# Kernel optimization log

Hardware: AMD Instinct MI355X
Metric: run time of the kernel (lower is better)

Reference implementation:

```python
import jax, jax.numpy as jnp
import numpy as np

ATTENTION_HEAD = 16
EXPANSION_LENGTH = 300
TEXT_EMBEDDING_DIM = 768
LN_EPS = 1e-3  # keras LayerNormalization default epsilon


def setup_inputs() -> dict:
    key = jax.random.key(0)
    ks = jax.random.split(key, 8)
    B, L, D = 8, 2048, TEXT_EMBEDDING_DIM
    H = ATTENTION_HEAD
    E = EXPANSION_LENGTH
    dh = D // H
    glorot = lambda k, shape, fan_in, fan_out: jax.random.uniform(
        k, shape, jnp.float32,
        -jnp.sqrt(6.0 / (fan_in + fan_out)), jnp.sqrt(6.0 / (fan_in + fan_out)))
    return {
        "q": jax.random.normal(ks[0], (B, 1, L, D), jnp.float32),
        "k": jax.random.normal(ks[1], (B, 1, L, D), jnp.float32),
        "v": jax.random.normal(ks[2], (B, 1, L, D), jnp.float32),
        "Wq": glorot(ks[3], (D, D), D, D),
        "bq": jnp.zeros((D,), jnp.float32),
        "Wv": glorot(ks[4], (D, D), D, D),
        "bv": jnp.zeros((D,), jnp.float32),
        "memory": glorot(ks[5], (E, H, dh), E, dh),
        "gamma": jnp.ones((D,), jnp.float32),
        "beta": jnp.zeros((D,), jnp.float32),
    }


def reference(q, k, v, Wq, bq, Wv, bv, memory, gamma, beta):
    B, _, L, D = q.shape
    H = ATTENTION_HEAD
    dh = D // H
    # Dense projections (v is unused by the original module)
    Q_ = q @ Wq + bq                      # (B,1,L,D)
    V_ = k @ Wv + bv                      # (B,1,L,D)
    Q = Q_.reshape(B, L, H, dh)
    V = V_.reshape(B, L, H, dh)
    # memory-query scores, ReLU instead of softmax
    eij = jax.nn.relu(jnp.einsum('ehd,blhd->belh', memory, Q))  # (B,E,L,H)
    out1 = jnp.einsum('belh,blhd->behd', eij, V)                # (B,E,H,dh)
    out2 = jnp.einsum('behd,belh->blhd', out1, eij)             # (B,L,H,dh)
    x = out2.reshape(B, 1, L, D)
    mean = jnp.mean(x, axis=-1, keepdims=True)
    var = jnp.var(x, axis=-1, keepdims=True)
    return (x - mean) * jax.lax.rsqrt(var + LN_EPS) * gamma + beta
```

## Files before the change

kernel.cpp:

```cpp
#include <hip/hip_runtime.h>
#include <hip/hip_bf16.h>
#include <stdint.h>

#define B_   8
#define L_   2048
#define D_   768
#define H_   16
#define DH   48
#define E_   300
#define EP   320
#define KP   64
#define ACH  4
#define N1T  (128 * DH * EP)

typedef __bf16 bf16;
typedef __bf16 bf16x8 __attribute__((ext_vector_type(8)));
typedef __bf16 bf16x4 __attribute__((ext_vector_type(4)));
typedef float  f32x4  __attribute__((ext_vector_type(4)));

typedef const __attribute__((address_space(1))) uint32_t guint;
typedef __attribute__((address_space(3))) uint32_t luint;

__device__ __forceinline__ f32x4 mfma16(bf16x8 a, bf16x8 b, f32x4 c) {
  return __builtin_amdgcn_mfma_f32_16x16x32_bf16(a, b, c, 0, 0, 0);
}

__global__ __launch_bounds__(256) void k_wt(const float* __restrict__ Wq,
                                            const float* __restrict__ Wv,
                                            bf16* __restrict__ WqT,
                                            bf16* __restrict__ WvT) {
  int idx = blockIdx.x * 256 + threadIdx.x;
  int n = idx / D_, k = idx % D_;
  const float* W = blockIdx.y ? Wv : Wq;
  bf16* WT = blockIdx.y ? WvT : WqT;
  WT[n * D_ + k] = (bf16)W[k * D_ + n];
}

__global__ __launch_bounds__(256) void k_mem(const float* __restrict__ M,
                                             bf16* __restrict__ MP) {
  int idx = blockIdx.x * 256 + threadIdx.x;
  int h = idx / (EP * KP);
  int r = idx % (EP * KP);
  int e = r / KP, d = r % KP;
  float v = (e < E_ && d < DH) ? M[(e * H_ + h) * DH + d] : 0.f;
  MP[idx] = (bf16)v;
}

__global__ __launch_bounds__(512, 4) void k_gemm(
    const float* __restrict__ A0, const float* __restrict__ A1,
    const bf16* __restrict__ WT0, const bf16* __restrict__ WT1,
    const float* __restrict__ b0, const float* __restrict__ b1,
    bf16* __restrict__ outQ, bf16* __restrict__ outVT) {
  __shared__ bf16 As[128 * 32];
  __shared__ bf16 Bs[256 * 32];
  const int tid = threadIdx.x, lane = tid & 63, w = tid >> 6;
  const int wr = w >> 2, wc = w & 3;
  const int lr = lane & 15, lq = lane >> 4;
  const int bid = blockIdx.x;
  const int j = (bid & 7) * 48 + (bid >> 3);
  const int n0 = (j % 3) * 256, m0 = (j / 3) * 128;
  const int mode = blockIdx.y;
  const float* A = mode ? A1 : A0;
  const bf16* WT = mode ? WT1 : WT0;
  const float* bias = mode ? b1 : b0;

  const int arow = tid >> 2, ac8 = tid & 3;
  const int aslot = ac8 ^ ((arow >> 1) & 3);

  f32x4 acc[4][4] = {};

  for (int k0 = 0; k0 < D_; k0 += 32) {
    __syncthreads();
    {
      const float* src = A + (size_t)(m0 + arow) * D_ + k0 + ac8 * 8;
      float4 f0 = *(const float4*)src;
      float4 f1 = *(const float4*)(src + 4);
      bf16x8 v;
      v[0] = (bf16)f0.x; v[1] = (bf16)f0.y; v[2] = (bf16)f0.z; v[3] = (bf16)f0.w;
      v[4] = (bf16)f1.x; v[5] = (bf16)f1.y; v[6] = (bf16)f1.z; v[7] = (bf16)f1.w;
      *(bf16x8*)&As[arow * 32 + aslot * 8] = v;
    }
#pragma unroll
    for (int t = 0; t < 2; ++t) {
      int idx = tid + t * 512;
      int brow = idx >> 2, bt = idx & 3;
      int bc8 = bt ^ ((brow >> 1) & 3);
      const bf16* src = WT + (size_t)(n0 + brow) * D_ + k0 + bc8 * 8;
      __builtin_amdgcn_global_load_lds((guint*)src,
                                       (luint*)&Bs[(t * 512 + w * 64) * 8], 16, 0, 0);
    }
    __syncthreads();
    bf16x8 af[4], bfr[4];
#pragma unroll
    for (int mi = 0; mi < 4; ++mi) {
      int row = wr * 64 + mi * 16 + lr;
      af[mi] = *(const bf16x8*)&As[row * 32 + (lq ^ ((row >> 1) & 3)) * 8];
    }
#pragma unroll
    for (int ni = 0; ni < 4; ++ni) {
      int row = wc * 64 + ni * 16 + lr;
      bfr[ni] = *(const bf16x8*)&Bs[row * 32 + (lq ^ ((row >> 1) & 3)) * 8];
    }
#pragma unroll
    for (int mi = 0; mi < 4; ++mi)
#pragma unroll
      for (int ni = 0; ni < 4; ++ni)
        acc[mi][ni] = mfma16(af[mi], bfr[ni], acc[mi][ni]);
  }

  float bs[4];
#pragma unroll
  for (int ni = 0; ni < 4; ++ni) bs[ni] = bias[n0 + wc * 64 + ni * 16 + lr];

  if (mode == 0) {
#pragma unroll
    for (int mi = 0; mi < 4; ++mi)
#pragma unroll
      for (int ni = 0; ni < 4; ++ni) {
        int m = m0 + wr * 64 + mi * 16 + lq * 4;
        int n = n0 + wc * 64 + ni * 16 + lr;
#pragma unroll
        for (int r = 0; r < 4; ++r)
          outQ[(size_t)(m + r) * D_ + n] = (bf16)(acc[mi][ni][r] + bs[ni]);
      }
  } else {
#pragma unroll
    for (int mi = 0; mi < 4; ++mi)
#pragma unroll
      for (int ni = 0; ni < 4; ++ni) {
        int mb = m0 + wr * 64 + mi * 16 + lq * 4;
        int n = n0 + wc * 64 + ni * 16 + lr;
        int bhd = (mb >> 11) * H_ + n / DH;
        int d = n % DH;
        int l = mb & (L_ - 1);
        bf16x4 v;
#pragma unroll
        for (int r = 0; r < 4; ++r) v[r] = (bf16)(acc[mi][ni][r] + bs[ni]);
        *(bf16x4*)&outVT[((size_t)bhd * DH + d) * L_ + l] = v;
      }
  }
}

__global__ __launch_bounds__(256) void k_phaseA(
    const bf16* __restrict__ Qb, const bf16* __restrict__ VT,
    const bf16* __restrict__ MP, float* __restrict__ O1P) {
  __shared__ bf16 Qs[2][32 * 88];
  __shared__ bf16 Vs[2][48 * 40];
  __shared__ bf16 Ss[EP * 40];
  const int tid = threadIdx.x, lane = tid & 63, w = tid >> 6;
  const int lr = lane & 15, lq = lane >> 4;
  const int bh = blockIdx.y, b = bh >> 4, h = bh & 15;
  const int lbase = blockIdx.x * (L_ / ACH);

  bf16x8 mf[5][2];
#pragma unroll
  for (int mi = 0; mi < 5; ++mi)
#pragma unroll
    for (int kh = 0; kh < 2; ++kh)
      mf[mi][kh] = *(const bf16x8*)&MP[(size_t)(h * EP + w * 80 + mi * 16 + lr) * KP + kh * 32 + lq * 8];

  if (tid < 128) {
    int buf = tid >> 6, t = tid & 63;
    uint4 z = {0, 0, 0, 0};
    *(uint4*)&Qs[buf][(t >> 1) * 88 + 48 + (t & 1) * 8] = z;
  }

  auto loadQ = [&](int idx, int l0) {
    return *(const bf16x8*)&Qb[(size_t)(b * L_ + l0 + idx / 6) * D_ + h * DH + (idx % 6) * 8];
  };
  auto loadV = [&](int j, int l0) {
    return *(const bf16x8*)&VT[((size_t)bh * DH + (j >> 2)) * L_ + l0 + (j & 3) * 8];
  };

  bf16x8 rA, rB;
  {
    int l0 = lbase;
    rA = (tid < 192) ? loadQ(tid, l0) : loadV(tid - 192, l0);
    if (tid < 128) rB = loadV(tid + 64, l0);
  }

  f32x4 acc[5][3] = {};

  for (int it = 0; it < L_ / ACH / 32; ++it) {
    const int cur = it & 1;
    if (tid < 192) *(bf16x8*)&Qs[cur][(tid / 6) * 88 + (tid % 6) * 8] = rA;
    else           *(bf16x8*)&Vs[cur][((tid - 192) >> 2) * 40 + ((tid - 192) & 3) * 8] = rA;
    if (tid < 128) *(bf16x8*)&Vs[cur][((tid + 64) >> 2) * 40 + ((tid + 64) & 3) * 8] = rB;
    __syncthreads();
    if (it + 1 < L_ / ACH / 32) {
      int l0 = lbase + (it + 1) * 32;
      rA = (tid < 192) ? loadQ(tid, l0) : loadV(tid - 192, l0);
      if (tid < 128) rB = loadV(tid + 64, l0);
    }
    bf16x8 qf[2][2];
#pragma unroll
    for (int ni = 0; ni < 2; ++ni)
#pragma unroll
      for (int kh = 0; kh < 2; ++kh)
        qf[ni][kh] = *(const bf16x8*)&Qs[cur][(ni * 16 + lr) * 88 + kh * 32 + lq * 8];
#pragma unroll
    for (int mi = 0; mi < 5; ++mi)
#pragma unroll
      for (int ni = 0; ni < 2; ++ni) {
        f32x4 s = {0.f, 0.f, 0.f, 0.f};
        s = mfma16(mf[mi][0], qf[ni][0], s);
        s = mfma16(mf[mi][1], qf[ni][1], s);
#pragma unroll
        for (int r = 0; r < 4; ++r)
          Ss[(w * 80 + mi * 16 + lq * 4 + r) * 40 + ni * 16 + lr] =
              (bf16)(s[r] > 0.f ? s[r] : 0.f);
      }
    bf16x8 sf[5], vf[3];
#pragma unroll
    for (int mi = 0; mi < 5; ++mi)
      sf[mi] = *(const bf16x8*)&Ss[(w * 80 + mi * 16 + lr) * 40 + lq * 8];
#pragma unroll
    for (int ni = 0; ni < 3; ++ni)
      vf[ni] = *(const bf16x8*)&Vs[cur][(ni * 16 + lr) * 40 + lq * 8];
#pragma unroll
    for (int mi = 0; mi < 5; ++mi)
#pragma unroll
      for (int ni = 0; ni < 3; ++ni)
        acc[mi][ni] = mfma16(sf[mi], vf[ni], acc[mi][ni]);
  }
  float* dst = O1P + (size_t)(blockIdx.x * 128 + bh) * DH * EP;
#pragma unroll
  for (int mi = 0; mi < 5; ++mi)
#pragma unroll
    for (int ni = 0; ni < 3; ++ni) {
      int e = w * 80 + mi * 16 + lq * 4;
      int d = ni * 16 + lr;
#pragma unroll
      for (int r = 0; r < 4; ++r)
        dst[(size_t)d * EP + e + r] = acc[mi][ni][r];
    }
}

__global__ __launch_bounds__(256) void k_red(const float* __restrict__ O1P,
                                             bf16* __restrict__ O1T) {
  int idx = blockIdx.x * 256 + threadIdx.x;
  if (idx >= N1T) return;
  float s = O1P[idx];
#pragma unroll
  for (int c = 1; c < ACH; ++c) s += O1P[(size_t)c * N1T + idx];
  O1T[idx] = (bf16)s;
}

__global__ __launch_bounds__(256, 4) void k_phaseB(
    const bf16* __restrict__ Qb, const bf16* __restrict__ MP,
    const bf16* __restrict__ O1T, bf16* __restrict__ X) {
  __shared__ bf16 Qs[64 * 88];
  __shared__ bf16 STs[64 * 76];
  __shared__ bf16 O1s[2][48 * 76];
  const int tid = threadIdx.x, lane = tid & 63, w = tid >> 6;
  const int lr = lane & 15, lq = lane >> 4;
  const int bh = blockIdx.y, b = bh >> 4, h = bh & 15;
  const int l0 = blockIdx.x * 64;

  bf16x8 mfB[5][2];
#pragma unroll
  for (int c = 0; c < 5; ++c)
#pragma unroll
    for (int kh = 0; kh < 2; ++kh)
      mfB[c][kh] = *(const bf16x8*)&MP[(size_t)(h * EP + c * 64 + w * 16 + lr) * KP + kh * 32 + lq * 8];

  for (int idx = tid; idx < 512; idx += 256) {
    if (idx < 384) {
      int row = idx / 6, c = idx % 6;
      *(bf16x8*)&Qs[row * 88 + c * 8] =
          *(const bf16x8*)&Qb[(size_t)(b * L_ + l0 + row) * D_ + h * DH + c * 8];
    } else {
      int j = idx - 384;
      uint4 z = {0, 0, 0, 0};
      *(uint4*)&Qs[(j >> 1) * 88 + 48 + (j & 1) * 8] = z;
    }
  }
  for (int idx = tid; idx < 384; idx += 256)
    *(bf16x8*)&O1s[0][(idx >> 3) * 76 + (idx & 7) * 8] =
        *(const bf16x8*)&O1T[((size_t)bh * DH + (idx >> 3)) * EP + (idx & 7) * 8];
  __syncthreads();

  f32x4 acc[3] = {};
#pragma unroll
  for (int c = 0; c < 5; ++c) {
    bf16x8 r0, r1;
    if (c < 4) {
      r0 = *(const bf16x8*)&O1T[((size_t)bh * DH + (tid >> 3)) * EP + (c + 1) * 64 + (tid & 7) * 8];
      if (tid < 128) {
        int i2 = tid + 256;
        r1 = *(const bf16x8*)&O1T[((size_t)bh * DH + (i2 >> 3)) * EP + (c + 1) * 64 + (i2 & 7) * 8];
      }
    }
#pragma unroll
    for (int mi = 0; mi < 4; ++mi) {
      bf16x8 qa0 = *(const bf16x8*)&Qs[(mi * 16 + lr) * 88 + lq * 8];
      bf16x8 qa1 = *(const bf16x8*)&Qs[(mi * 16 + lr) * 88 + 32 + lq * 8];
      f32x4 s = {0.f, 0.f, 0.f, 0.f};
      s = mfma16(qa0, mfB[c][0], s);
      s = mfma16(qa1, mfB[c][1], s);
#pragma unroll
      for (int r = 0; r < 4; ++r)
        STs[(mi * 16 + lq * 4 + r) * 76 + w * 16 + lr] =
            (bf16)(s[r] > 0.f ? s[r] : 0.f);
    }
    __syncthreads();
#pragma unroll
    for (int ks = 0; ks < 2; ++ks) {
      bf16x8 sf = *(const bf16x8*)&STs[(w * 16 + lr) * 76 + ks * 32 + lq * 8];
#pragma unroll
      for (int ni = 0; ni < 3; ++ni) {
        bf16x8 of = *(const bf16x8*)&O1s[c & 1][(ni * 16 + lr) * 76 + ks * 32 + lq * 8];
        acc[ni] = mfma16(sf, of, acc[ni]);
      }
    }
    if (c < 4) {
      *(bf16x8*)&O1s[(c + 1) & 1][(tid >> 3) * 76 + (tid & 7) * 8] = r0;
      if (tid < 128) {
        int i2 = tid + 256;
        *(bf16x8*)&O1s[(c + 1) & 1][(i2 >> 3) * 76 + (i2 & 7) * 8] = r1;
      }
    }
    __syncthreads();
  }
#pragma unroll
  for (int ni = 0; ni < 3; ++ni)
#pragma unroll
    for (int r = 0; r < 4; ++r)
      X[(size_t)(b * L_ + l0 + w * 16 + lq * 4 + r) * D_ + h * DH + ni * 16 + lr] =
          (bf16)acc[ni][r];
}

__global__ __launch_bounds__(256) void k_ln(
    const bf16* __restrict__ X, const float* __restrict__ gamma,
    const float* __restrict__ beta, float* __restrict__ out) {
  const int lane = threadIdx.x & 63;
  const int row = blockIdx.x * 4 + (threadIdx.x >> 6);
  const bf16* x = X + (size_t)row * D_;
  float v[12];
#pragma unroll
  for (int c = 0; c < 3; ++c) {
    bf16x4 ch = *(const bf16x4*)(x + lane * 12 + c * 4);
#pragma unroll
    for (int j = 0; j < 4; ++j) v[c * 4 + j] = (float)ch[j];
  }
  float s = 0.f, q = 0.f;
#pragma unroll
  for (int j = 0; j < 12; ++j) { s += v[j]; q += v[j] * v[j]; }
#pragma unroll
  for (int off = 32; off > 0; off >>= 1) {
    s += __shfl_xor(s, off);
    q += __shfl_xor(q, off);
  }
  float mean = s * (1.f / 768.f);
  float var = q * (1.f / 768.f) - mean * mean;
  float inv = rsqrtf(var + 1e-3f);
  float* o = out + (size_t)row * D_;
#pragma unroll
  for (int c = 0; c < 3; ++c) {
    float4 g = *(const float4*)(gamma + lane * 12 + c * 4);
    float4 bt = *(const float4*)(beta + lane * 12 + c * 4);
    float4 r;
    r.x = (v[c * 4 + 0] - mean) * inv * g.x + bt.x;
    r.y = (v[c * 4 + 1] - mean) * inv * g.y + bt.y;
    r.z = (v[c * 4 + 2] - mean) * inv * g.z + bt.z;
    r.w = (v[c * 4 + 3] - mean) * inv * g.w + bt.w;
    *(float4*)(o + lane * 12 + c * 4) = r;
  }
}

extern "C" void kernel_launch(void* const* d_in, const int* in_sizes, int n_in,
                              void* d_out, int out_size, void* d_ws, size_t ws_size,
                              hipStream_t stream) {
  (void)in_sizes; (void)n_in; (void)out_size; (void)ws_size;
  const float* q_in = (const float*)d_in[0];
  const float* k_in = (const float*)d_in[1];
  const float* Wq   = (const float*)d_in[3];
  const float* bq   = (const float*)d_in[4];
  const float* Wv   = (const float*)d_in[5];
  const float* bv   = (const float*)d_in[6];
  const float* mem  = (const float*)d_in[7];
  const float* gam  = (const float*)d_in[8];
  const float* bet  = (const float*)d_in[9];
  float* out = (float*)d_out;

  char* ws = (char*)d_ws;
  size_t off = 0;
  auto alloc = [&](size_t bytes) {
    char* p = ws + off;
    off += (bytes + 255) & ~(size_t)255;
    return p;
  };
  bf16*  WqT = (bf16*)alloc((size_t)D_ * D_ * 2);
  bf16*  WvT = (bf16*)alloc((size_t)D_ * D_ * 2);
  bf16*  MP  = (bf16*)alloc((size_t)H_ * EP * KP * 2);
  bf16*  Qb  = (bf16*)alloc((size_t)B_ * L_ * D_ * 2);
  bf16*  VT  = (bf16*)alloc((size_t)B_ * H_ * DH * L_ * 2);
  bf16*  O1T = (bf16*)alloc((size_t)N1T * 2);
  const size_t o1pBytes = (size_t)ACH * N1T * 4;
  const size_t xbBytes  = (size_t)B_ * L_ * D_ * 2;
  char*  big = alloc(xbBytes > o1pBytes ? xbBytes : o1pBytes);
  float* O1P = (float*)big;
  bf16*  Xb  = (bf16*)big;

  k_wt<<<dim3((D_ * D_) / 256, 2), 256, 0, stream>>>(Wq, Wv, WqT, WvT);
  k_mem<<<(H_ * EP * KP) / 256, 256, 0, stream>>>(mem, MP);
  k_gemm<<<dim3(384, 2), 512, 0, stream>>>(q_in, k_in, WqT, WvT, bq, bv, Qb, VT);
  k_phaseA<<<dim3(ACH, B_ * H_), 256, 0, stream>>>(Qb, VT, MP, O1P);
  k_red<<<(N1T + 255) / 256, 256, 0, stream>>>(O1P, O1T);
  k_phaseB<<<dim3(L_ / 64, B_ * H_), 256, 0, stream>>>(Qb, MP, O1T, Xb);
  k_ln<<<(B_ * L_) / 4, 256, 0, stream>>>(Xb, gam, bet, out);
}
```

Baseline: 175.7 us.

## Double-buffer the projection GEMM k-loop with register and LDS prefetch

The projection GEMM now uses two LDS buffers for the A and B tiles. The next k-slice is prefetched while the current one is consumed: A goes into registers and B goes into the alternate LDS buffer via global_load_lds. This removes one barrier per iteration and overlaps global load latency with MFMA work. In exchange, LDS use per block doubles, which may reduce how many blocks fit on each CU.

Measured after the change: 178.2 us. About the same (+1.4%).

```diff
diff --git a/kernel.cpp b/kernel.cpp
--- a/kernel.cpp
+++ b/kernel.cpp
@@ -12,6 +12,7 @@
 #define KP   64
 #define ACH  4
 #define N1T  (128 * DH * EP)
+#define NT_  24
 
 typedef __bf16 bf16;
 typedef __bf16 bf16x8 __attribute__((ext_vector_type(8)));
@@ -51,8 +52,8 @@
     const bf16* __restrict__ WT0, const bf16* __restrict__ WT1,
     const float* __restrict__ b0, const float* __restrict__ b1,
     bf16* __restrict__ outQ, bf16* __restrict__ outVT) {
-  __shared__ bf16 As[128 * 32];
-  __shared__ bf16 Bs[256 * 32];
+  __shared__ bf16 As[2][128 * 32];
+  __shared__ bf16 Bs[2][256 * 32];
   const int tid = threadIdx.x, lane = tid & 63, w = tid >> 6;
   const int wr = w >> 2, wc = w & 3;
   const int lr = lane & 15, lq = lane >> 4;
@@ -66,20 +67,11 @@
 
   const int arow = tid >> 2, ac8 = tid & 3;
   const int aslot = ac8 ^ ((arow >> 1) & 3);
+  const float* aSrc = A + (size_t)(m0 + arow) * D_ + ac8 * 8;
 
   f32x4 acc[4][4] = {};
 
-  for (int k0 = 0; k0 < D_; k0 += 32) {
-    __syncthreads();
-    {
-      const float* src = A + (size_t)(m0 + arow) * D_ + k0 + ac8 * 8;
-      float4 f0 = *(const float4*)src;
-      float4 f1 = *(const float4*)(src + 4);
-      bf16x8 v;
-      v[0] = (bf16)f0.x; v[1] = (bf16)f0.y; v[2] = (bf16)f0.z; v[3] = (bf16)f0.w;
-      v[4] = (bf16)f1.x; v[5] = (bf16)f1.y; v[6] = (bf16)f1.z; v[7] = (bf16)f1.w;
-      *(bf16x8*)&As[arow * 32 + aslot * 8] = v;
-    }
+  auto stageB = [&](int buf, int k0) {
 #pragma unroll
     for (int t = 0; t < 2; ++t) {
       int idx = tid + t * 512;
@@ -87,19 +79,39 @@
       int bc8 = bt ^ ((brow >> 1) & 3);
       const bf16* src = WT + (size_t)(n0 + brow) * D_ + k0 + bc8 * 8;
       __builtin_amdgcn_global_load_lds((guint*)src,
-                                       (luint*)&Bs[(t * 512 + w * 64) * 8], 16, 0, 0);
+                                       (luint*)&Bs[buf][(t * 512 + w * 64) * 8], 16, 0, 0);
+    }
+  };
+
+  float4 f0 = *(const float4*)(aSrc);
+  float4 f1 = *(const float4*)(aSrc + 4);
+  stageB(0, 0);
+
+  for (int t = 0; t < NT_; ++t) {
+    const int cur = t & 1;
+    {
+      bf16x8 v;
+      v[0] = (bf16)f0.x; v[1] = (bf16)f0.y; v[2] = (bf16)f0.z; v[3] = (bf16)f0.w;
+      v[4] = (bf16)f1.x; v[5] = (bf16)f1.y; v[6] = (bf16)f1.z; v[7] = (bf16)f1.w;
+      *(bf16x8*)&As[cur][arow * 32 + aslot * 8] = v;
     }
     __syncthreads();
+    if (t + 1 < NT_) {
+      const float* s = aSrc + (t + 1) * 32;
+      f0 = *(const float4*)s;
+      f1 = *(const float4*)(s + 4);
+      stageB(cur ^ 1, (t + 1) * 32);
+    }
     bf16x8 af[4], bfr[4];
 #pragma unroll
     for (int mi = 0; mi < 4; ++mi) {
       int row = wr * 64 + mi * 16 + lr;
-      af[mi] = *(const bf16x8*)&As[row * 32 + (lq ^ ((row >> 1) & 3)) * 8];
+      af[mi] = *(const bf16x8*)&As[cur][row * 32 + (lq ^ ((row >> 1) & 3)) * 8];
     }
 #pragma unroll
     for (int ni = 0; ni < 4; ++ni) {
       int row = wc * 64 + ni * 16 + lr;
-      bfr[ni] = *(const bf16x8*)&Bs[row * 32 + (lq ^ ((row >> 1) & 3)) * 8];
+      bfr[ni] = *(const bf16x8*)&Bs[cur][row * 32 + (lq ^ ((row >> 1) & 3)) * 8];
     }
 #pragma unroll
     for (int mi = 0; mi < 4; ++mi)
```

## Triple-buffer GEMM K-loop with async LDS loads of fp32 A tiles

Applied to the files above, without the earlier changes.

The projection GEMM now keeps a three-stage ring of LDS buffers. Both the fp32 A tile and the bf16 weight tile are fetched with global_load_lds two iterations ahead, using vmcnt waits and a single barrier per step. Conversion of A to bf16 moves from the global-load path to the LDS read, so LDS holds fp32 A (double the bytes) and occupancy drops to two blocks per SM via launch bounds. The goal is to overlap global latency with MFMA work, at the cost of more LDS traffic and lower occupancy.

Measured after the change: 205.2 us. +16.8%, slower.

```diff
diff --git a/kernel.cpp b/kernel.cpp
--- a/kernel.cpp
+++ b/kernel.cpp
@@ -12,6 +12,7 @@
 #define KP   64
 #define ACH  4
 #define N1T  (128 * DH * EP)
+#define NT_  24
 
 typedef __bf16 bf16;
 typedef __bf16 bf16x8 __attribute__((ext_vector_type(8)));
@@ -46,13 +47,13 @@
   MP[idx] = (bf16)v;
 }
 
-__global__ __launch_bounds__(512, 4) void k_gemm(
+__global__ __launch_bounds__(512, 2) void k_gemm(
     const float* __restrict__ A0, const float* __restrict__ A1,
     const bf16* __restrict__ WT0, const bf16* __restrict__ WT1,
     const float* __restrict__ b0, const float* __restrict__ b1,
     bf16* __restrict__ outQ, bf16* __restrict__ outVT) {
-  __shared__ bf16 As[128 * 32];
-  __shared__ bf16 Bs[256 * 32];
+  __shared__ float Asf[3][128 * 32];
+  __shared__ bf16  Bs[3][256 * 32];
   const int tid = threadIdx.x, lane = tid & 63, w = tid >> 6;
   const int wr = w >> 2, wc = w & 3;
   const int lr = lane & 15, lq = lane >> 4;
@@ -64,42 +65,58 @@
   const bf16* WT = mode ? WT1 : WT0;
   const float* bias = mode ? b1 : b0;
 
-  const int arow = tid >> 2, ac8 = tid & 3;
-  const int aslot = ac8 ^ ((arow >> 1) & 3);
-
-  f32x4 acc[4][4] = {};
-
-  for (int k0 = 0; k0 < D_; k0 += 32) {
-    __syncthreads();
-    {
-      const float* src = A + (size_t)(m0 + arow) * D_ + k0 + ac8 * 8;
-      float4 f0 = *(const float4*)src;
-      float4 f1 = *(const float4*)(src + 4);
-      bf16x8 v;
-      v[0] = (bf16)f0.x; v[1] = (bf16)f0.y; v[2] = (bf16)f0.z; v[3] = (bf16)f0.w;
-      v[4] = (bf16)f1.x; v[5] = (bf16)f1.y; v[6] = (bf16)f1.z; v[7] = (bf16)f1.w;
-      *(bf16x8*)&As[arow * 32 + aslot * 8] = v;
-    }
+  auto stage = [&](int buf, int k0) {
 #pragma unroll
     for (int t = 0; t < 2; ++t) {
       int idx = tid + t * 512;
-      int brow = idx >> 2, bt = idx & 3;
-      int bc8 = bt ^ ((brow >> 1) & 3);
-      const bf16* src = WT + (size_t)(n0 + brow) * D_ + k0 + bc8 * 8;
+      int row = idx >> 3, s4 = idx & 7;
+      int g4 = s4 ^ ((row >> 1) & 7);
+      const float* src = A + (size_t)(m0 + row) * D_ + k0 + g4 * 4;
       __builtin_amdgcn_global_load_lds((guint*)src,
-                                       (luint*)&Bs[(t * 512 + w * 64) * 8], 16, 0, 0);
-    }
-    __syncthreads();
+          (luint*)&Asf[buf][(t * 512 + w * 64) * 4], 16, 0, 0);
+    }
+#pragma unroll
+    for (int t = 0; t < 2; ++t) {
+      int idx = tid + t * 512;
+      int row = idx >> 2, s8 = idx & 3;
+      int g8 = s8 ^ ((row >> 1) & 3);
+      const bf16* src = WT + (size_t)(n0 + row) * D_ + k0 + g8 * 8;
+      __builtin_amdgcn_global_load_lds((guint*)src,
+          (luint*)&Bs[buf][(t * 512 + w * 64) * 8], 16, 0, 0);
+    }
+  };
+
+  f32x4 acc[4][4] = {};
+
+  stage(0, 0);
+  stage(1, 32);
+
+  for (int t = 0; t < NT_; ++t) {
+    const int cur = t % 3;
+    if (t + 1 < NT_)
+      asm volatile("s_waitcnt vmcnt(4) lgkmcnt(0)" ::: "memory");
+    else
+      asm volatile("s_waitcnt vmcnt(0) lgkmcnt(0)" ::: "memory");
+    __builtin_amdgcn_s_barrier();
+    __builtin_amdgcn_sched_barrier(0);
+    if (t + 2 < NT_) stage((t + 2) % 3, (t + 2) * 32);
+
     bf16x8 af[4], bfr[4];
 #pragma unroll
     for (int mi = 0; mi < 4; ++mi) {
       int row = wr * 64 + mi * 16 + lr;
-      af[mi] = *(const bf16x8*)&As[row * 32 + (lq ^ ((row >> 1) & 3)) * 8];
+      int sw = (row >> 1) & 7;
+      float4 p0 = *(const float4*)&Asf[cur][row * 32 + (((lq * 2) ^ sw) * 4)];
+      float4 p1 = *(const float4*)&Asf[cur][row * 32 + (((lq * 2 + 1) ^ sw) * 4)];
+      bf16x8 v;
+      v[0] = (bf16)p0.x; v[1] = (bf16)p0.y; v[2] = (bf16)p0.z; v[3] = (bf16)p0.w;
+      v[4] = (bf16)p1.x; v[5] = (bf16)p1.y; v[6] = (bf16)p1.z; v[7] = (bf16)p1.w;
+      af[mi] = v;
     }
 #pragma unroll
     for (int ni = 0; ni < 4; ++ni) {
       int row = wc * 64 + ni * 16 + lr;
-      bfr[ni] = *(const bf16x8*)&Bs[row * 32 + (lq ^ ((row >> 1) & 3)) * 8];
+      bfr[ni] = *(const bf16x8*)&Bs[cur][row * 32 + ((lq ^ ((row >> 1) & 3)) * 8)];
     }
 #pragma unroll
     for (int mi = 0; mi < 4; ++mi)
```
